# Performance work log

Measured on AMD Instinct MI355X. Metric: run time of the kernel, lower is better.

## Reference

```python
import jax, jax.numpy as jnp
import numpy as np

B, T, V, E, DC, H = 128, 25, 10000, 512, 512, 512
N0 = H + E + DC  # layer-0 concat width
N1 = 2 * H       # layer-1 concat width


def setup_inputs() -> dict:
    key = jax.random.key(0)
    ks = jax.random.split(key, 12)
    def w(k, n):
        return jax.random.normal(k, (n, H), dtype=jnp.float32) / np.float32(np.sqrt(n))
    return {
        "tokens": jax.random.randint(ks[0], (B, T), 0, V),
        "processed_cnn_features": jax.random.normal(ks[1], (B, DC), dtype=jnp.float32),
        "initial_hidden_state": jnp.zeros((2, B, H), dtype=jnp.float32),
        "embedding": jax.random.normal(ks[2], (V, E), dtype=jnp.float32) * 0.1,
        "Wu0": w(ks[3], N0), "Wr0": w(ks[4], N0), "Wc0": w(ks[5], N0),
        "bu0": jnp.zeros((H,), jnp.float32), "br0": jnp.zeros((H,), jnp.float32), "bc0": jnp.zeros((H,), jnp.float32),
        "Wu1": w(ks[6], N1), "Wr1": w(ks[7], N1), "Wc1": w(ks[8], N1),
        "bu1": jnp.zeros((H,), jnp.float32), "br1": jnp.zeros((H,), jnp.float32), "bc1": jnp.zeros((H,), jnp.float32),
        "Wout": jax.random.normal(ks[9], (H, V), dtype=jnp.float32) / np.float32(np.sqrt(H)),
        "bout": jnp.zeros((V,), jnp.float32),
    }


def gru_step(x, h, Wu, bu, Wr, br, Wc, bc):
    xh = jnp.concatenate([x, h], axis=1)
    u = jax.nn.sigmoid(xh @ Wu + bu)
    r = jax.nn.sigmoid(xh @ Wr + br)
    cand = jnp.tanh(jnp.concatenate([x, r * h], axis=1) @ Wc + bc)
    return u * h + (1.0 - u) * cand


def reference(tokens, processed_cnn_features, initial_hidden_state, embedding,
              Wu0, Wr0, Wc0, bu0, br0, bc0,
              Wu1, Wr1, Wc1, bu1, br1, bc1,
              Wout, bout):
    emb = embedding[tokens]              # [B, T, E]
    emb_t = jnp.transpose(emb, (1, 0, 2))  # [T, B, E]

    def step(carry, e_t):
        h0, h1 = carry
        x0 = jnp.concatenate([e_t, processed_cnn_features], axis=1)  # [B, E+DC]
        h0 = gru_step(x0, h0, Wu0, bu0, Wr0, br0, Wc0, bc0)
        h1 = gru_step(h0, h1, Wu1, bu1, Wr1, br1, Wc1, bc1)
        logits = h1 @ Wout + bout  # [B, V]
        return (h0, h1), logits

    (h0, h1), logits_seq = jax.lax.scan(step, (initial_hidden_state[0], initial_hidden_state[1]), emb_t)
    logits = jnp.transpose(logits_seq, (1, 0, 2))  # [B, T, V]
    final_hidden = jnp.stack([h0, h1])             # [2, B, H]
    return logits, final_hidden
```

## Files before the change

### kernel.cpp

```cpp
#include <hip/hip_runtime.h>

#define T_ 25
#define V_ 10000
#define NWG_ 192
#define NGRP_ 16
#define GSZ_ (NWG_ / NGRP_)

typedef short bf16x8 __attribute__((ext_vector_type(8)));
typedef float f32x4 __attribute__((ext_vector_type(4)));

__device__ __forceinline__ short f2bf(float x) {
  union { float f; unsigned u; } v; v.f = x;
  unsigned r = (v.u + 0x7fffu + ((v.u >> 16) & 1u)) >> 16;
  return (short)r;
}
__device__ __forceinline__ float sigm(float z) { return 1.f / (1.f + __expf(-z)); }
__device__ __forceinline__ float tanhfast(float z) {
  float e = __expf(2.f * z);
  return 1.f - 2.f / (e + 1.f);
}

__device__ __forceinline__ void gload_lds16(const void* g, void* l) {
  __builtin_amdgcn_global_load_lds((const __attribute__((address_space(1))) void*)g,
                                   (__attribute__((address_space(3))) void*)l, 16, 0, 0);
}

__device__ __forceinline__ void vwait0() { asm volatile("s_waitcnt vmcnt(0)" ::: "memory"); }
__device__ __forceinline__ void vwait_n(int n) {
  switch (n) {
    case 0:  asm volatile("s_waitcnt vmcnt(0)"  ::: "memory"); break;
    case 8:  asm volatile("s_waitcnt vmcnt(8)"  ::: "memory"); break;
    case 16: asm volatile("s_waitcnt vmcnt(16)" ::: "memory"); break;
    default: asm volatile("s_waitcnt vmcnt(0)"  ::: "memory"); break;
  }
}
__device__ __forceinline__ void cload16(bf16x8* d, const short* p) {
  asm volatile("global_load_dwordx4 %0, %1, off sc0 sc1" : "=v"(*d) : "v"(p) : "memory");
}
__device__ __forceinline__ void cloadf(float* d, const float* p) {
  asm volatile("global_load_dword %0, %1, off sc0 sc1" : "=v"(*d) : "v"(p) : "memory");
}
__device__ __forceinline__ void cstoref(float* p, float v) {
  asm volatile("global_store_dword %0, %1, off sc0 sc1" :: "v"(p), "v"(v) : "memory");
}
__device__ __forceinline__ void cstores(short* p, int v) {
  asm volatile("global_store_short %0, %1, off sc0 sc1" :: "v"(p), "v"(v) : "memory");
}

__device__ __forceinline__ int FL(int row, int col) {
  return (((col >> 5) * 8 + (row >> 4)) << 9) | (((row & 15) | (((col >> 3) & 3) << 4)) << 3) | (col & 7);
}

__device__ __forceinline__ void gbar(int* bar, int gen) {
  vwait0();
  __syncthreads();
  if (threadIdx.x == 0) {
    __hip_atomic_fetch_add(&bar[(blockIdx.x & (NGRP_ - 1)) * 32], 1,
                           __ATOMIC_RELAXED, __HIP_MEMORY_SCOPE_AGENT);
    const int need = gen * GSZ_;
    int sweeps = 0;
    for (;;) {
      int mn = 0x7fffffff;
#pragma unroll
      for (int i = 0; i < NGRP_; i++) {
        int v = __hip_atomic_load(&bar[i * 32], __ATOMIC_RELAXED, __HIP_MEMORY_SCOPE_AGENT);
        mn = v < mn ? v : mn;
      }
      if (mn >= need) break;
      if ((++sweeps & 63) == 0)
        (void)__hip_atomic_load(&bar[0], __ATOMIC_ACQUIRE, __HIP_MEMORY_SCOPE_AGENT);
      __builtin_amdgcn_s_sleep(1);
    }
  }
  __syncthreads();
}

struct TJob { const float* src; short* dst; int R, C, t0; };
struct TJobs { TJob j[10]; };

__global__ void tcast_all(TJobs J) {
  __shared__ float t[32][33];
  int bid = blockIdx.x;
  int ji = 0;
  while (ji < 9 && bid >= J.j[ji + 1].t0) ji++;
  const float* src = J.j[ji].src;
  short* dst = J.j[ji].dst;
  int R = J.j[ji].R, C = J.j[ji].C;
  int rel = bid - J.j[ji].t0;
  int ctiles = (C + 31) >> 5;
  int rt0 = (rel / ctiles) * 32, ct0 = (rel % ctiles) * 32;
  int tx = threadIdx.x, ty = threadIdx.y;
#pragma unroll
  for (int i = 0; i < 4; i++) {
    int r = rt0 + ty + i * 8, c = ct0 + tx;
    if (r < R && c < C) t[ty + i * 8][tx] = src[(size_t)r * C + c];
  }
  __syncthreads();
#pragma unroll
  for (int i = 0; i < 4; i++) {
    int c = ct0 + ty + i * 8, r = rt0 + tx;
    if (r < R && c < C) dst[(size_t)c * R + r] = f2bf(t[tx][ty + i * 8]);
  }
}

__global__ void build_x0(const int* __restrict__ tok, const float* __restrict__ emb,
                         const float* __restrict__ cnn, short* __restrict__ X0) {
  int row = blockIdx.x;
  int t = row >> 7, b = row & 127;
  int tk = tok[b * T_ + t];
  const float* er = emb + (size_t)tk * 512;
  short* dst = X0 + (size_t)row * 1024;
  for (int i = threadIdx.x; i < 1024; i += 256)
    dst[i] = f2bf(i < 512 ? er[i] : cnn[b * 512 + (i - 512)]);
}

__global__ void init_h(const float* __restrict__ ihs, float* h0f, float* h1f, short* xh1b) {
  int i = blockIdx.x * 256 + threadIdx.x;
  if (i < 65536) {
    int b = i >> 9, h = i & 511;
    float v0 = ihs[i], v1 = ihs[65536 + i];
    h0f[i] = v0; h1f[i] = v1;
    xh1b[FL(b, h)] = f2bf(v0);
    xh1b[FL(b, 512 + h)] = f2bf(v1);
  }
}

struct RP {
  short *xh1b, *rh0b, *xc1b0, *xc1b1, *H1all;
  float *u0f, *u1f, *h0f, *h1f;
  const float *A0;
  const short *Whur0T, *Whc0T, *W1urT, *Wc1T;
  const float *bu1, *br1, *bc1;
  float *outp;
  int *bar;
};

template<int NKS>
__device__ __forceinline__ void wload(const short* __restrict__ Wt, int n0, int lane, bf16x8* wfr) {
  const short* p = Wt + (size_t)(n0 + (lane & 15)) * (NKS * 32) + ((lane >> 4) * 8);
#pragma unroll
  for (int ks = 0; ks < NKS; ks++) wfr[ks] = *(const bf16x8*)(p + (size_t)ks * 32);
}

template<int NKS>
__device__ __forceinline__ void kcompute_coh(const short* __restrict__ A, int rb0, int lane,
                                             const bf16x8* __restrict__ wfr, f32x4* acc) {
  const short* ap = A + rb0 * 512 + lane * 8;
  constexpr int NCH = NKS / 4;
  constexpr int DEPTH = NCH < 3 ? NCH : 3;
  bf16x8 s0[4][4], s1[4][4];
#pragma unroll
  for (int c = 0; c < DEPTH; c++)
#pragma unroll
    for (int j = 0; j < 4; j++) {
      cload16(&s0[c & 3][j], ap + (c * 4 + j) * 4096);
      cload16(&s1[c & 3][j], ap + (c * 4 + j) * 4096 + 512);
    }
#pragma unroll
  for (int c = 0; c < NCH; c++) {
    const int issued = (DEPTH + c < NCH) ? DEPTH + c : NCH;
    vwait_n((issued - c - 1) * 8);
    __builtin_amdgcn_sched_barrier(0);
#pragma unroll
    for (int j = 0; j < 4; j++) {
      int ks = c * 4 + j;
      acc[ks & 1]       = __builtin_amdgcn_mfma_f32_16x16x32_bf16(s0[c & 3][j], wfr[ks], acc[ks & 1], 0, 0, 0);
      acc[2 + (ks & 1)] = __builtin_amdgcn_mfma_f32_16x16x32_bf16(s1[c & 3][j], wfr[ks], acc[2 + (ks & 1)], 0, 0, 0);
    }
    if (DEPTH + c < NCH) {
      const int nc = DEPTH + c;
#pragma unroll
      for (int j = 0; j < 4; j++) {
        cload16(&s0[nc & 3][j], ap + (nc * 4 + j) * 4096);
        cload16(&s1[nc & 3][j], ap + (nc * 4 + j) * 4096 + 512);
      }
    }
  }
}

__global__ __launch_bounds__(256, 1) void recurrence(RP p) {
  const int role = blockIdx.x;
  const int tid = threadIdx.x, wv = tid >> 6, lane = tid & 63;
  const int lr = lane & 15, lg = lane >> 4;
  int gen = 0;

  if (role < 64) {
    const int nt = role >> 1, mh = role & 1;
    const int colb = nt * 32 + (wv & 1) * 16;
    const int rb0 = mh * 4 + (wv >> 1) * 2;
    const int col = colb + lr;
    bf16x8 wfr[32]; wload<32>(p.W1urT, colb, lane, wfr);
    gbar(p.bar, ++gen); gbar(p.bar, ++gen);
    for (int t = 0; t < T_; t++) {
      float hv[8];
      if (colb >= 512) {
#pragma unroll
        for (int m = 0; m < 2; m++)
#pragma unroll
          for (int i = 0; i < 4; i++)
            cloadf(&hv[m * 4 + i], &p.h1f[((rb0 + m) * 16 + lg * 4 + i) * 512 + (col - 512)]);
      }
      f32x4 acc[4] = {};
      kcompute_coh<32>(p.xh1b, rb0, lane, wfr, acc);
      f32x4 am[2] = { acc[0] + acc[1], acc[2] + acc[3] };
      short* xc = (t & 1) ? p.xc1b1 : p.xc1b0;
      if (colb < 512) {
#pragma unroll
        for (int m = 0; m < 2; m++)
#pragma unroll
          for (int i = 0; i < 4; i++) {
            int row = (rb0 + m) * 16 + lg * 4 + i;
            cstoref(&p.u1f[row * 512 + col], sigm(am[m][i] + p.bu1[col]));
          }
      } else {
#pragma unroll
        for (int m = 0; m < 2; m++)
#pragma unroll
          for (int i = 0; i < 4; i++) {
            int row = (rb0 + m) * 16 + lg * 4 + i;
            float s = sigm(am[m][i] + p.br1[col - 512]);
            cstores(&xc[FL(row, col)], f2bf(s * hv[m * 4 + i]));
          }
      }
      gbar(p.bar, ++gen);
      gbar(p.bar, ++gen);
    }
  } else if (role < 128) {
    const int r2 = role - 64;
    const int nt = r2 >> 1, mh = r2 & 1;
    const int colb = nt * 32 + (wv & 1) * 16;
    const int rb0 = mh * 4 + (wv >> 1) * 2;
    const int col = colb + lr;
    bf16x8 wfr[16]; wload<16>(p.Whur0T, colb, lane, wfr);
    auto doP1 = [&](int tt) {
      float hv[8];
      if (colb >= 512) {
#pragma unroll
        for (int m = 0; m < 2; m++)
#pragma unroll
          for (int i = 0; i < 4; i++)
            cloadf(&hv[m * 4 + i], &p.h0f[((rb0 + m) * 16 + lg * 4 + i) * 512 + (col - 512)]);
      }
      f32x4 acc[4] = {};
      kcompute_coh<16>(p.xh1b, rb0, lane, wfr, acc);
      f32x4 am[2] = { acc[0] + acc[1], acc[2] + acc[3] };
      const float* a0s = p.A0 + (size_t)tt * 196608;
      if (colb < 512) {
#pragma unroll
        for (int m = 0; m < 2; m++)
#pragma unroll
          for (int i = 0; i < 4; i++) {
            int row = (rb0 + m) * 16 + lg * 4 + i;
            cstoref(&p.u0f[row * 512 + col], sigm(am[m][i] + a0s[row * 1536 + col]));
          }
      } else {
#pragma unroll
        for (int m = 0; m < 2; m++)
#pragma unroll
          for (int i = 0; i < 4; i++) {
            int row = (rb0 + m) * 16 + lg * 4 + i;
            float s = sigm(am[m][i] + a0s[row * 1536 + col]);
            cstores(&p.rh0b[FL(row, col - 512)], f2bf(s * hv[m * 4 + i]));
          }
      }
    };
    doP1(0);
    gbar(p.bar, ++gen); gbar(p.bar, ++gen);
    for (int t = 0; t < T_; t++) {
      if (t < T_ - 1) doP1(t + 1);
      gbar(p.bar, ++gen);
      gbar(p.bar, ++gen);
    }
  } else if (role < 160) {
    const int r4 = role - 128;
    const int nt = r4 >> 1, mh = r4 & 1;
    const int colb = nt * 32 + (wv & 1) * 16;
    const int rb0 = mh * 4 + (wv >> 1) * 2;
    const int col = colb + lr;
    bf16x8 wfr[32]; wload<32>(p.Wc1T, colb, lane, wfr);
    gbar(p.bar, ++gen); gbar(p.bar, ++gen);
    for (int t = 0; t < T_; t++) {
      gbar(p.bar, ++gen);
      const short* xc = (t & 1) ? p.xc1b1 : p.xc1b0;
      float uv[8], hv[8];
#pragma unroll
      for (int m = 0; m < 2; m++)
#pragma unroll
        for (int i = 0; i < 4; i++) {
          int row = (rb0 + m) * 16 + lg * 4 + i;
          cloadf(&uv[m * 4 + i], &p.u1f[row * 512 + col]);
          cloadf(&hv[m * 4 + i], &p.h1f[row * 512 + col]);
        }
      f32x4 acc[4] = {};
      kcompute_coh<32>(xc, rb0, lane, wfr, acc);
      f32x4 am[2] = { acc[0] + acc[1], acc[2] + acc[3] };
#pragma unroll
      for (int m = 0; m < 2; m++)
#pragma unroll
        for (int i = 0; i < 4; i++) {
          int row = (rb0 + m) * 16 + lg * 4 + i;
          float cc = tanhfast(am[m][i] + p.bc1[col]);
          float u = uv[m * 4 + i], h = hv[m * 4 + i];
          float hn = u * h + (1.f - u) * cc;
          cstoref(&p.h1f[row * 512 + col], hn);
          short hb = f2bf(hn);
          cstores(&p.xh1b[FL(row, 512 + col)], hb);
          p.H1all[(size_t)t * 65536 + row * 512 + col] = hb;
          if (t == T_ - 1) p.outp[32000000 + 65536 + row * 512 + col] = hn;
        }
      gbar(p.bar, ++gen);
    }
  } else {
    const int r2 = role - 160;
    const int nt = r2 >> 1, mh = r2 & 1;
    const int colb = nt * 32 + (wv & 1) * 16;
    const int rb0 = mh * 4 + (wv >> 1) * 2;
    const int col = colb + lr;
    bf16x8 wfr[16]; wload<16>(p.Whc0T, colb, lane, wfr);
    auto doP2 = [&](int tt) {
      float uv[8], hv[8];
#pragma unroll
      for (int m = 0; m < 2; m++)
#pragma unroll
        for (int i = 0; i < 4; i++) {
          int row = (rb0 + m) * 16 + lg * 4 + i;
          cloadf(&uv[m * 4 + i], &p.u0f[row * 512 + col]);
          cloadf(&hv[m * 4 + i], &p.h0f[row * 512 + col]);
        }
      f32x4 acc[4] = {};
      kcompute_coh<16>(p.rh0b, rb0, lane, wfr, acc);
      f32x4 am[2] = { acc[0] + acc[1], acc[2] + acc[3] };
      const float* a0s = p.A0 + (size_t)tt * 196608;
      short* xcw = (tt & 1) ? p.xc1b1 : p.xc1b0;
#pragma unroll
      for (int m = 0; m < 2; m++)
#pragma unroll
        for (int i = 0; i < 4; i++) {
          int row = (rb0 + m) * 16 + lg * 4 + i;
          float c = tanhfast(am[m][i] + a0s[row * 1536 + 1024 + col]);
          float u = uv[m * 4 + i], h = hv[m * 4 + i];
          float hn = u * h + (1.f - u) * c;
          cstoref(&p.h0f[row * 512 + col], hn);
          short hb = f2bf(hn);
          cstores(&p.xh1b[FL(row, col)], hb);
          cstores(&xcw[FL(row, col)], hb);
          if (tt == T_ - 1) p.outp[32000000 + row * 512 + col] = hn;
        }
    };
    gbar(p.bar, ++gen);
    doP2(0);
    gbar(p.bar, ++gen);
    for (int t = 0; t < T_; t++) {
      gbar(p.bar, ++gen);
      if (t < T_ - 1) doP2(t + 1);
      gbar(p.bar, ++gen);
    }
  }
}

struct GP {
  const short* A; const short* Bt;
  int lda, ldb, N, K;
  const float* bias0; const float* bias1; const float* bias2;
  float* fdst;
  float* outp; const float* bout;
};

template<int BM, int BN, int VAR>
__device__ __forceinline__ void gemm_core(const GP& p, short* la, short* lb, int bm, int bn, short* smem) {
  const int tid = threadIdx.x;
  const int wave = tid >> 6, lane = tid & 63;
  const int wm = wave >> 1, wn = wave & 1;
  constexpr int WM = BM / 2, WN = BN / 2;
  constexpr int MF = WM / 16, NF = WN / 16;
  const int lr = lane & 15, lg = lane >> 4;
  const short* Abase = p.A + (size_t)bm * BM * p.lda;
  const short* Bbase = p.Bt + (size_t)bn * BN * p.ldb;
  const int bnmax = p.N - bn * BN;
  f32x4 acc[MF][NF] = {};
  const int nkb = p.K >> 6;

  auto stA = [&](int buf, int k0) {
    constexpr int NI = BM / 32;
#pragma unroll
    for (int j = 0; j < NI; j++) {
      int glin = j * 256 + tid;
      int row = glin >> 3, gc = glin & 7;
      int gcs = gc ^ (row & 7);
      gload_lds16(Abase + (size_t)row * p.lda + k0 + gcs * 8,
                  &la[buf * BM * 64 + j * 2048 + wave * 512]);
    }
  };
  auto stB = [&](int buf, int k0) {
    constexpr int NI = BN / 32;
#pragma unroll
    for (int j = 0; j < NI; j++) {
      int glin = j * 256 + tid;
      int row = glin >> 3, gc = glin & 7;
      int gcs = gc ^ (row & 7);
      int rc = row < bnmax ? row : bnmax - 1;
      gload_lds16(Bbase + (size_t)rc * p.ldb + k0 + gcs * 8,
                  &lb[buf * BN * 64 + j * 2048 + wave * 512]);
    }
  };

  stA(0, 0); stB(0, 0);
  __syncthreads();
  int buf = 0;
  for (int kb = 0; kb < nkb; kb++) {
    if (kb + 1 < nkb) { stA(buf ^ 1, (kb + 1) * 64); stB(buf ^ 1, (kb + 1) * 64); }
    bf16x8 af[2][MF], bfr[2][NF];
#pragma unroll
    for (int ks = 0; ks < 2; ks++) {
#pragma unroll
      for (int m = 0; m < MF; m++) {
        int ar = wm * WM + m * 16 + lr;
        af[ks][m] = *(const bf16x8*)&la[buf * BM * 64 + (ar * 8 + ((ks * 4 + lg) ^ (ar & 7))) * 8];
      }
#pragma unroll
      for (int n = 0; n < NF; n++) {
        int br = wn * WN + n * 16 + lr;
        bfr[ks][n] = *(const bf16x8*)&lb[buf * BN * 64 + (br * 8 + ((ks * 4 + lg) ^ (br & 7))) * 8];
      }
    }
#pragma unroll
    for (int ks = 0; ks < 2; ks++)
#pragma unroll
      for (int m = 0; m < MF; m++)
#pragma unroll
        for (int n = 0; n < NF; n++)
          acc[m][n] = __builtin_amdgcn_mfma_f32_16x16x32_bf16(af[ks][m], bfr[ks][n], acc[m][n], 0, 0, 0);
    __syncthreads();
    buf ^= 1;
  }

  if constexpr (VAR == 0) {
#pragma unroll
    for (int m = 0; m < MF; m++)
#pragma unroll
      for (int n = 0; n < NF; n++)
#pragma unroll
        for (int i = 0; i < 4; i++) {
          int row = bm * BM + wm * WM + m * 16 + lg * 4 + i;
          int col = bn * BN + wn * WN + n * 16 + lr;
          if (col >= p.N) continue;
          float bias = col < 512 ? p.bias0[col] : (col < 1024 ? p.bias1[col - 512] : p.bias2[col - 1024]);
          p.fdst[(size_t)row * 1536 + col] = acc[m][n][i] + bias;
        }
  } else {
    float* fs = (float*)smem;
#pragma unroll
    for (int m = 0; m < MF; m++)
#pragma unroll
      for (int n = 0; n < NF; n++)
#pragma unroll
        for (int i = 0; i < 4; i++) {
          int lrow = wm * WM + m * 16 + lg * 4 + i;
          int lcol = wn * WN + n * 16 + lr;
          int col = bn * BN + lcol;
          fs[lrow * 128 + lcol] = acc[m][n][i] + (col < p.N ? p.bout[col] : 0.f);
        }
    __syncthreads();
#pragma unroll
    for (int j = 0; j < 16; j++) {
      int idx = j * 256 + tid;
      int r = idx >> 5, c4 = (idx & 31) << 2;
      int gr = bm * BM + r;
      int tt = gr >> 7, b = gr & 127;
      int col = bn * BN + c4;
      if (col < p.N) {
        f32x4 v = *(const f32x4*)&fs[r * 128 + c4];
        *(f32x4*)&p.outp[((size_t)b * T_ + tt) * V_ + col] = v;
      }
    }
  }
}

template<int BM, int BN, int VAR>
__global__ __launch_bounds__(256) void gemm_one(GP p) {
  __shared__ short smem[2 * BM * 64 + 2 * BN * 64];
  int bm, bn;
  if constexpr (VAR == 5) {
    int lin = blockIdx.y * gridDim.x + blockIdx.x;
    const int nwg = 79 * 25, q = nwg / 8, r8 = nwg % 8;
    int xcd = lin % 8, idx = lin / 8;
    int nlin = (xcd < r8 ? xcd * (q + 1) : r8 * (q + 1) + (xcd - r8) * q) + idx;
    bm = nlin % 25; bn = nlin / 25;
  } else { bm = blockIdx.y; bn = blockIdx.x; }
  gemm_core<BM, BN, VAR>(p, smem, smem + 2 * BM * 64, bm, bn, smem);
}

extern "C" void kernel_launch(void* const* d_in, const int* in_sizes, int n_in,
                              void* d_out, int out_size, void* d_ws, size_t ws_size,
                              hipStream_t stream) {
  const int*   tokens = (const int*)  d_in[0];
  const float* cnn    = (const float*)d_in[1];
  const float* ihs    = (const float*)d_in[2];
  const float* emb    = (const float*)d_in[3];
  const float* Wu0 = (const float*)d_in[4];
  const float* Wr0 = (const float*)d_in[5];
  const float* Wc0 = (const float*)d_in[6];
  const float* bu0 = (const float*)d_in[7];
  const float* br0 = (const float*)d_in[8];
  const float* bc0 = (const float*)d_in[9];
  const float* Wu1 = (const float*)d_in[10];
  const float* Wr1 = (const float*)d_in[11];
  const float* Wc1 = (const float*)d_in[12];
  const float* bu1 = (const float*)d_in[13];
  const float* br1 = (const float*)d_in[14];
  const float* bc1 = (const float*)d_in[15];
  const float* Wout = (const float*)d_in[16];
  const float* bout = (const float*)d_in[17];
  float* out = (float*)d_out;

  char* w = (char*)d_ws;
  size_t off = 0;
  auto alloc = [&](size_t bytes) { void* p = w + off; off += (bytes + 255) & ~255ull; return p; };
  short* WxT    = (short*)alloc(1536 * 1024 * 2);
  short* Whur0T = (short*)alloc(1024 * 512 * 2);
  short* Whc0T  = (short*)alloc(512 * 512 * 2);
  short* W1urT  = (short*)alloc(1024 * 1024 * 2);
  short* Wc1T   = (short*)alloc(512 * 1024 * 2);
  short* WoutT  = (short*)alloc((size_t)10000 * 512 * 2);
  short* X0     = (short*)alloc((size_t)3200 * 1024 * 2);
  float* A0     = (float*)alloc((size_t)3200 * 1536 * 4);
  short* H1all  = (short*)alloc((size_t)3200 * 512 * 2);
  float* u0f    = (float*)alloc(128 * 512 * 4);
  float* u1f    = (float*)alloc(128 * 512 * 4);
  float* h0f    = (float*)alloc(128 * 512 * 4);
  float* h1f    = (float*)alloc(128 * 512 * 4);
  short* rh0b   = (short*)alloc(128 * 512 * 2);
  short* xh1b   = (short*)alloc(128 * 1024 * 2);
  short* xc1b0  = (short*)alloc(128 * 1024 * 2);
  short* xc1b1  = (short*)alloc(128 * 1024 * 2);
  int*   bar    = (int*)alloc(4096);
  (void)ws_size; (void)in_sizes; (void)n_in; (void)out_size;

  {
    TJobs J;
    J.j[0] = { Wu0,              WxT,                1024, 512,  0    };
    J.j[1] = { Wr0,              WxT + 512 * 1024,   1024, 512,  512  };
    J.j[2] = { Wc0,              WxT + 1024 * 1024,  1024, 512,  1024 };
    J.j[3] = { Wu0 + 1024 * 512, Whur0T,             512,  512,  1536 };
    J.j[4] = { Wr0 + 1024 * 512, Whur0T + 512 * 512, 512,  512,  1792 };
    J.j[5] = { Wc0 + 1024 * 512, Whc0T,              512,  512,  2048 };
    J.j[6] = { Wu1,              W1urT,              1024, 512,  2304 };
    J.j[7] = { Wr1,              W1urT + 512 * 1024, 1024, 512,  2816 };
    J.j[8] = { Wc1,              Wc1T,               1024, 512,  3328 };
    J.j[9] = { Wout,             WoutT,              512,  10000, 3840 };
    tcast_all<<<8848, dim3(32, 8), 0, stream>>>(J);
  }

  build_x0<<<3200, 256, 0, stream>>>(tokens, emb, cnn, X0);
  init_h<<<256, 256, 0, stream>>>(ihs, h0f, h1f, xh1b);
  hipMemsetAsync(bar, 0, 4096, stream);

  {
    GP g = {};
    g.A = X0; g.lda = 1024; g.Bt = WxT; g.ldb = 1024; g.N = 1536; g.K = 1024;
    g.bias0 = bu0; g.bias1 = br0; g.bias2 = bc0; g.fdst = A0;
    gemm_one<128, 128, 0><<<dim3(12, 25), 256, 0, stream>>>(g);
  }

  {
    RP r = {};
    r.xh1b = xh1b; r.rh0b = rh0b; r.xc1b0 = xc1b0; r.xc1b1 = xc1b1; r.H1all = H1all;
    r.u0f = u0f; r.u1f = u1f; r.h0f = h0f; r.h1f = h1f;
    r.A0 = A0;
    r.Whur0T = Whur0T; r.Whc0T = Whc0T; r.W1urT = W1urT; r.Wc1T = Wc1T;
    r.bu1 = bu1; r.br1 = br1; r.bc1 = bc1;
    r.outp = out;
    r.bar = bar;
    recurrence<<<dim3(NWG_), 256, 0, stream>>>(r);
  }

  {
    GP g = {};
    g.A = H1all; g.lda = 512; g.Bt = WoutT; g.ldb = 512; g.N = 10000; g.K = 512;
    g.outp = out; g.bout = bout;
    gemm_one<128, 128, 5><<<dim3(79, 25), 256, 0, stream>>>(g);
  }
}
```

Baseline: 583.6 us.

## Replace global grid barriers with per-role dataflow counters and double-buffered state

Swaps the all-workgroup generation barrier in the persistent GRU recurrence for per-phase arrival counters. Each role now waits only on the specific producer phases it depends on. The shared xh1b buffer becomes double-buffered so layer-0 and layer-1 phases of adjacent timesteps can overlap without write-after-read hazards. This is meant to cut barrier latency and let phases pipeline across timesteps, at the cost of more complex dependency counts that must be exactly right to avoid races.

```diff
diff --git a/kernel.cpp b/kernel.cpp
--- a/kernel.cpp
+++ b/kernel.cpp
@@ -3,8 +3,11 @@
 #define T_ 25
 #define V_ 10000
 #define NWG_ 192
-#define NGRP_ 16
-#define GSZ_ (NWG_ / NGRP_)
+
+#define R_P1 0
+#define R_P2 1
+#define R_P3 2
+#define R_P4 3
 
 typedef short bf16x8 __attribute__((ext_vector_type(8)));
 typedef float f32x4 __attribute__((ext_vector_type(4)));
@@ -51,25 +54,28 @@
   return (((col >> 5) * 8 + (row >> 4)) << 9) | (((row & 15) | (((col >> 3) & 3) << 4)) << 3) | (col & 7);
 }
 
-__device__ __forceinline__ void gbar(int* bar, int gen) {
+__device__ __forceinline__ void arrive(int* bar, int role, int rep) {
   vwait0();
   __syncthreads();
+  if (threadIdx.x == 0)
+    __hip_atomic_fetch_add(&bar[(role * 8 + rep) * 32], 1, __ATOMIC_RELAXED, __HIP_MEMORY_SCOPE_AGENT);
+}
+__device__ __forceinline__ int rsum(int* bar, int role) {
+  int s = 0;
+#pragma unroll
+  for (int r = 0; r < 8; r++)
+    s += __hip_atomic_load(&bar[(role * 8 + r) * 32], __ATOMIC_RELAXED, __HIP_MEMORY_SCOPE_AGENT);
+  return s;
+}
+__device__ __forceinline__ void waitc(int* bar, int r0, int n0, int r1, int n1, int r2, int n2) {
   if (threadIdx.x == 0) {
-    __hip_atomic_fetch_add(&bar[(blockIdx.x & (NGRP_ - 1)) * 32], 1,
-                           __ATOMIC_RELAXED, __HIP_MEMORY_SCOPE_AGENT);
-    const int need = gen * GSZ_;
-    int sweeps = 0;
     for (;;) {
-      int mn = 0x7fffffff;
-#pragma unroll
-      for (int i = 0; i < NGRP_; i++) {
-        int v = __hip_atomic_load(&bar[i * 32], __ATOMIC_RELAXED, __HIP_MEMORY_SCOPE_AGENT);
-        mn = v < mn ? v : mn;
-      }
-      if (mn >= need) break;
-      if ((++sweeps & 63) == 0)
-        (void)__hip_atomic_load(&bar[0], __ATOMIC_ACQUIRE, __HIP_MEMORY_SCOPE_AGENT);
-      __builtin_amdgcn_s_sleep(1);
+      bool ok = true;
+      if (r0 >= 0 && rsum(bar, r0) < n0) ok = false;
+      if (ok && r1 >= 0 && rsum(bar, r1) < n1) ok = false;
+      if (ok && r2 >= 0 && rsum(bar, r2) < n2) ok = false;
+      if (ok) break;
+      __builtin_amdgcn_s_sleep(2);
     }
   }
   __syncthreads();
@@ -114,19 +120,20 @@
     dst[i] = f2bf(i < 512 ? er[i] : cnn[b * 512 + (i - 512)]);
 }
 
-__global__ void init_h(const float* __restrict__ ihs, float* h0f, float* h1f, short* xh1b) {
+__global__ void init_h(const float* __restrict__ ihs, float* h0f, float* h1f,
+                       short* xh1b0, short* xh1b1) {
   int i = blockIdx.x * 256 + threadIdx.x;
   if (i < 65536) {
     int b = i >> 9, h = i & 511;
     float v0 = ihs[i], v1 = ihs[65536 + i];
     h0f[i] = v0; h1f[i] = v1;
-    xh1b[FL(b, h)] = f2bf(v0);
-    xh1b[FL(b, 512 + h)] = f2bf(v1);
+    xh1b1[FL(b, h)] = f2bf(v0);
+    xh1b0[FL(b, 512 + h)] = f2bf(v1);
   }
 }
 
 struct RP {
-  short *xh1b, *rh0b, *xc1b0, *xc1b1, *H1all;
+  short *xh1b0, *xh1b1, *rh0b, *xc1b0, *xc1b1, *H1all;
   float *u0f, *u1f, *h0f, *h1f;
   const float *A0;
   const short *Whur0T, *Whc0T, *W1urT, *Wc1T;
@@ -182,16 +189,18 @@
   const int role = blockIdx.x;
   const int tid = threadIdx.x, wv = tid >> 6, lane = tid & 63;
   const int lr = lane & 15, lg = lane >> 4;
-  int gen = 0;
+  int* bar = p.bar;
 
   if (role < 64) {
-    const int nt = role >> 1, mh = role & 1;
+    const int widx = role, rep = widx & 7;
+    const int nt = widx >> 1, mh = widx & 1;
     const int colb = nt * 32 + (wv & 1) * 16;
     const int rb0 = mh * 4 + (wv >> 1) * 2;
     const int col = colb + lr;
     bf16x8 wfr[32]; wload<32>(p.W1urT, colb, lane, wfr);
-    gbar(p.bar, ++gen); gbar(p.bar, ++gen);
-    for (int t = 0; t < T_; t++) {
+    for (int s = 0; s < T_; s++) {
+      waitc(bar, R_P2, 32 * (s + 1), s >= 1 ? R_P4 : -1, 32 * s, -1, 0);
+      const short* A = (s & 1) ? p.xh1b1 : p.xh1b0;
       float hv[8];
       if (colb >= 512) {
 #pragma unroll
@@ -201,9 +210,9 @@
             cloadf(&hv[m * 4 + i], &p.h1f[((rb0 + m) * 16 + lg * 4 + i) * 512 + (col - 512)]);
       }
       f32x4 acc[4] = {};
-      kcompute_coh<32>(p.xh1b, rb0, lane, wfr, acc);
+      kcompute_coh<32>(A, rb0, lane, wfr, acc);
       f32x4 am[2] = { acc[0] + acc[1], acc[2] + acc[3] };
-      short* xc = (t & 1) ? p.xc1b1 : p.xc1b0;
+      short* xc = (s & 1) ? p.xc1b1 : p.xc1b0;
       if (colb < 512) {
 #pragma unroll
         for (int m = 0; m < 2; m++)
@@ -218,21 +227,22 @@
 #pragma unroll
           for (int i = 0; i < 4; i++) {
             int row = (rb0 + m) * 16 + lg * 4 + i;
-            float s = sigm(am[m][i] + p.br1[col - 512]);
-            cstores(&xc[FL(row, col)], f2bf(s * hv[m * 4 + i]));
+            float sg = sigm(am[m][i] + p.br1[col - 512]);
+            cstores(&xc[FL(row, col)], f2bf(sg * hv[m * 4 + i]));
           }
       }
-      gbar(p.bar, ++gen);
-      gbar(p.bar, ++gen);
+      arrive(bar, R_P3, rep);
     }
   } else if (role < 128) {
-    const int r2 = role - 64;
-    const int nt = r2 >> 1, mh = r2 & 1;
+    const int widx = role - 64, rep = widx & 7;
+    const int nt = widx >> 1, mh = widx & 1;
     const int colb = nt * 32 + (wv & 1) * 16;
     const int rb0 = mh * 4 + (wv >> 1) * 2;
     const int col = colb + lr;
     bf16x8 wfr[16]; wload<16>(p.Whur0T, colb, lane, wfr);
-    auto doP1 = [&](int tt) {
+    for (int s = 0; s < T_; s++) {
+      waitc(bar, s >= 1 ? R_P2 : -1, 32 * s, -1, 0, -1, 0);
+      const short* A = (s & 1) ? p.xh1b0 : p.xh1b1;
       float hv[8];
       if (colb >= 512) {
 #pragma unroll
@@ -242,9 +252,9 @@
             cloadf(&hv[m * 4 + i], &p.h0f[((rb0 + m) * 16 + lg * 4 + i) * 512 + (col - 512)]);
       }
       f32x4 acc[4] = {};
-      kcompute_coh<16>(p.xh1b, rb0, lane, wfr, acc);
+      kcompute_coh<16>(A, rb0, lane, wfr, acc);
       f32x4 am[2] = { acc[0] + acc[1], acc[2] + acc[3] };
-      const float* a0s = p.A0 + (size_t)tt * 196608;
+      const float* a0s = p.A0 + (size_t)s * 196608;
       if (colb < 512) {
 #pragma unroll
         for (int m = 0; m < 2; m++)
@@ -259,29 +269,22 @@
 #pragma unroll
           for (int i = 0; i < 4; i++) {
             int row = (rb0 + m) * 16 + lg * 4 + i;
-            float s = sigm(am[m][i] + a0s[row * 1536 + col]);
-            cstores(&p.rh0b[FL(row, col - 512)], f2bf(s * hv[m * 4 + i]));
+            float sg = sigm(am[m][i] + a0s[row * 1536 + col]);
+            cstores(&p.rh0b[FL(row, col - 512)], f2bf(sg * hv[m * 4 + i]));
           }
       }
-    };
-    doP1(0);
-    gbar(p.bar, ++gen); gbar(p.bar, ++gen);
-    for (int t = 0; t < T_; t++) {
-      if (t < T_ - 1) doP1(t + 1);
-      gbar(p.bar, ++gen);
-      gbar(p.bar, ++gen);
+      arrive(bar, R_P1, rep);
     }
   } else if (role < 160) {
-    const int r4 = role - 128;
-    const int nt = r4 >> 1, mh = r4 & 1;
+    const int widx = role - 128, rep = widx & 7;
+    const int nt = widx >> 1, mh = widx & 1;
     const int colb = nt * 32 + (wv & 1) * 16;
     const int rb0 = mh * 4 + (wv >> 1) * 2;
     const int col = colb + lr;
     bf16x8 wfr[32]; wload<32>(p.Wc1T, colb, lane, wfr);
-    gbar(p.bar, ++gen); gbar(p.bar, ++gen);
-    for (int t = 0; t < T_; t++) {
-      gbar(p.bar, ++gen);
-      const short* xc = (t & 1) ? p.xc1b1 : p.xc1b0;
+    for (int s = 0; s < T_; s++) {
+      waitc(bar, R_P3, 64 * (s + 1), R_P2, 32 * (s + 1), -1, 0);
+      const short* xc = (s & 1) ? p.xc1b1 : p.xc1b0;
       float uv[8], hv[8];
 #pragma unroll
       for (int m = 0; m < 2; m++)
@@ -294,6 +297,7 @@
       f32x4 acc[4] = {};
       kcompute_coh<32>(xc, rb0, lane, wfr, acc);
       f32x4 am[2] = { acc[0] + acc[1], acc[2] + acc[3] };
+      short* xh = (s & 1) ? p.xh1b0 : p.xh1b1;
 #pragma unroll
       for (int m = 0; m < 2; m++)
 #pragma unroll
@@ -304,20 +308,22 @@
           float hn = u * h + (1.f - u) * cc;
           cstoref(&p.h1f[row * 512 + col], hn);
           short hb = f2bf(hn);
-          cstores(&p.xh1b[FL(row, 512 + col)], hb);
-          p.H1all[(size_t)t * 65536 + row * 512 + col] = hb;
-          if (t == T_ - 1) p.outp[32000000 + 65536 + row * 512 + col] = hn;
+          cstores(&xh[FL(row, 512 + col)], hb);
+          p.H1all[(size_t)s * 65536 + row * 512 + col] = hb;
+          if (s == T_ - 1) p.outp[32000000 + 65536 + row * 512 + col] = hn;
         }
-      gbar(p.bar, ++gen);
+      arrive(bar, R_P4, rep);
     }
   } else {
-    const int r2 = role - 160;
-    const int nt = r2 >> 1, mh = r2 & 1;
+    const int widx = role - 160, rep = widx & 7;
+    const int nt = widx >> 1, mh = widx & 1;
     const int colb = nt * 32 + (wv & 1) * 16;
     const int rb0 = mh * 4 + (wv >> 1) * 2;
     const int col = colb + lr;
     bf16x8 wfr[16]; wload<16>(p.Whc0T, colb, lane, wfr);
-    auto doP2 = [&](int tt) {
+    for (int s = 0; s < T_; s++) {
+      waitc(bar, R_P1, 64 * (s + 1), s >= 1 ? R_P3 : -1, 64 * (s - 1),
+            s >= 2 ? R_P4 : -1, 32 * (s - 1));
       float uv[8], hv[8];
 #pragma unroll
       for (int m = 0; m < 2; m++)
@@ -330,8 +336,9 @@
       f32x4 acc[4] = {};
       kcompute_coh<16>(p.rh0b, rb0, lane, wfr, acc);
       f32x4 am[2] = { acc[0] + acc[1], acc[2] + acc[3] };
-      const float* a0s = p.A0 + (size_t)tt * 196608;
-      short* xcw = (tt & 1) ? p.xc1b1 : p.xc1b0;
+      const float* a0s = p.A0 + (size_t)s * 196608;
+      short* xh  = (s & 1) ? p.xh1b1 : p.xh1b0;
+      short* xcw = (s & 1) ? p.xc1b1 : p.xc1b0;
 #pragma unroll
       for (int m = 0; m < 2; m++)
 #pragma unroll
@@ -342,18 +349,11 @@
           float hn = u * h + (1.f - u) * c;
           cstoref(&p.h0f[row * 512 + col], hn);
           short hb = f2bf(hn);
-          cstores(&p.xh1b[FL(row, col)], hb);
+          cstores(&xh[FL(row, col)], hb);
           cstores(&xcw[FL(row, col)], hb);
-          if (tt == T_ - 1) p.outp[32000000 + row * 512 + col] = hn;
+          if (s == T_ - 1) p.outp[32000000 + row * 512 + col] = hn;
         }
-    };
-    gbar(p.bar, ++gen);
-    doP2(0);
-    gbar(p.bar, ++gen);
-    for (int t = 0; t < T_; t++) {
-      gbar(p.bar, ++gen);
-      if (t < T_ - 1) doP2(t + 1);
-      gbar(p.bar, ++gen);
+      arrive(bar, R_P2, rep);
     }
   }
 }
@@ -530,7 +530,8 @@
   float* h0f    = (float*)alloc(128 * 512 * 4);
   float* h1f    = (float*)alloc(128 * 512 * 4);
   short* rh0b   = (short*)alloc(128 * 512 * 2);
-  short* xh1b   = (short*)alloc(128 * 1024 * 2);
+  short* xh1b0  = (short*)alloc(128 * 1024 * 2);
+  short* xh1b1  = (short*)alloc(128 * 1024 * 2);
   short* xc1b0  = (short*)alloc(128 * 1024 * 2);
   short* xc1b1  = (short*)alloc(128 * 1024 * 2);
   int*   bar    = (int*)alloc(4096);
@@ -552,7 +553,7 @@
   }
 
   build_x0<<<3200, 256, 0, stream>>>(tokens, emb, cnn, X0);
-  init_h<<<256, 256, 0, stream>>>(ihs, h0f, h1f, xh1b);
+  init_h<<<256, 256, 0, stream>>>(ihs, h0f, h1f, xh1b0, xh1b1);
   hipMemsetAsync(bar, 0, 4096, stream);
 
   {
@@ -564,7 +565,8 @@
 
   {
     RP r = {};
-    r.xh1b = xh1b; r.rh0b = rh0b; r.xc1b0 = xc1b0; r.xc1b1 = xc1b1; r.H1all = H1all;
+    r.xh1b0 = xh1b0; r.xh1b1 = xh1b1; r.rh0b = rh0b; r.xc1b0 = xc1b0; r.xc1b1 = xc1b1;
+    r.H1all = H1all;
     r.u0f = u0f; r.u1f = u1f; r.h0f = h0f; r.h1f = h1f;
     r.A0 = A0;
     r.Whur0T = Whur0T; r.Whc0T = Whc0T; r.W1urT = W1urT; r.Wc1T = Wc1T;
```

Measured after the change: 548.9 us. 5.9% less time.
